# Kernel tuning notes

Hardware: AMD Instinct MI355X
Metric: run time of the kernel (lower is better)

## Reference

```python
import jax, jax.numpy as jnp
import numpy as np

DEPTH = 2
DIM = 256
MLP = 1024
B = 2
N = 2048


def setup_inputs() -> dict:
    key = jax.random.key(0)
    ks = jax.random.split(key, 6)
    s = 0.02
    d = DIM
    f32 = jnp.float32
    return {
        "x": jax.random.normal(ks[0], (B, N, d), f32),
        "ln1_g": jnp.ones((DEPTH, d), f32),
        "ln1_b": jnp.zeros((DEPTH, d), f32),
        "Wqkv": (jax.random.normal(ks[1], (DEPTH, d, 3 * d), f32) * s),
        "bqkv": jnp.zeros((DEPTH, 3 * d), f32),
        "Wo": (jax.random.normal(ks[2], (DEPTH, d, d), f32) * s),
        "bo": jnp.zeros((DEPTH, d), f32),
        "ln2_g": jnp.ones((DEPTH, d), f32),
        "ln2_b": jnp.zeros((DEPTH, d), f32),
        "W1": (jax.random.normal(ks[3], (DEPTH, d, MLP), f32) * s),
        "b1": jnp.zeros((DEPTH, MLP), f32),
        "W2": (jax.random.normal(ks[4], (DEPTH, MLP, d), f32) * s),
        "b2": jnp.zeros((DEPTH, d), f32),
        "heads": 8,
    }


def _ln(x, g, b, eps=1e-5):
    m = x.mean(-1, keepdims=True)
    v = ((x - m) ** 2).mean(-1, keepdims=True)
    return (x - m) * jax.lax.rsqrt(v + eps) * g + b


def reference(x, ln1_g, ln1_b, Wqkv, bqkv, Wo, bo, ln2_g, ln2_b, W1, b1, W2, b2, heads):
    b, n, dim = x.shape
    hd = dim // heads
    scale = hd ** -0.5
    depth = Wqkv.shape[0]
    out = x
    # NOTE: faithful to original: `x` is never updated inside the loop,
    # so only the last layer's output is returned.
    for i in range(depth):
        y = _ln(x, ln1_g[i], ln1_b[i])
        qkv = y @ Wqkv[i] + bqkv[i]                      # [b,n,3*dim]
        qkv = qkv.reshape(b, n, 3, heads, hd)
        q, k, v = jnp.moveaxis(qkv, 2, 0)                # each [b,n,h,hd]
        q = q.transpose(0, 2, 1, 3)                      # [b,h,n,hd]
        k = k.transpose(0, 2, 1, 3)
        v = v.transpose(0, 2, 1, 3)
        dots = jnp.einsum('bhid,bhjd->bhij', q, k) * scale
        attn = jax.nn.softmax(dots, axis=-1)
        o = jnp.einsum('bhij,bhjd->bhid', attn, v)       # [b,h,n,hd]
        o = o.transpose(0, 2, 1, 3).reshape(b, n, dim)
        o = o @ Wo[i] + bo[i]
        a = o + x                                        # attn residual
        z = _ln(a, ln2_g[i], ln2_b[i])
        m = jax.nn.gelu(z @ W1[i] + b1[i], approximate=False) @ W2[i] + b2[i]
        out = m + a                                      # mlp residual
    return out
```

## Files before the change

kernel.cpp:

```cpp
#include <hip/hip_runtime.h>
#include <hip/hip_bf16.h>
#include <math.h>

#define DEPTHC 2
#define DIMD   256
#define MLPD   1024
#define BB     2
#define NN     2048
#define HH     8
#define HD     32
#define ROWS   (BB * NN)

typedef __attribute__((ext_vector_type(8))) short bf16x8;
typedef __attribute__((ext_vector_type(4))) float f32x4;

__device__ __forceinline__ short f2bf(float x) {
    union { float f; unsigned u; } c; c.f = x;
    unsigned u = c.u + (0x7fffu + ((c.u >> 16) & 1u));
    return (short)(u >> 16);
}
__device__ __forceinline__ float bf2f(short s) {
    union { unsigned u; float f; } c; c.u = ((unsigned)(unsigned short)s) << 16;
    return c.f;
}

__global__ __launch_bounds__(256) void prep(
    const float* __restrict__ Wqkv, const float* __restrict__ Wo,
    const float* __restrict__ W1,   const float* __restrict__ W2,
    short* __restrict__ WqkvF, short* __restrict__ WoF,
    short* __restrict__ W1F,   short* __restrict__ W2F,
    const float* __restrict__ x, const float* __restrict__ g,
    const float* __restrict__ be, short* __restrict__ y)
{
    __shared__ short Ts[128][72];

    if (blockIdx.x >= 96) {
        const int wave = threadIdx.x >> 6;
        const int lane = threadIdx.x & 63;
        const int row  = (blockIdx.x - 96) * 4 + wave;
        const int c    = lane * 4;

        const float4 v = *(const float4*)&x[(size_t)row * DIMD + c];
        float s  = v.x + v.y + v.z + v.w;
        float sq = v.x * v.x + v.y * v.y + v.z * v.z + v.w * v.w;
#pragma unroll
        for (int off = 32; off > 0; off >>= 1) {
            s  += __shfl_down(s,  off, 64);
            sq += __shfl_down(sq, off, 64);
        }
        s  = __shfl(s,  0, 64);
        sq = __shfl(sq, 0, 64);

        const float mean = s * (1.f / DIMD);
        const float var  = sq * (1.f / DIMD) - mean * mean;
        const float rstd = rsqrtf(var + 1e-5f);

        const float4 gg = *(const float4*)&g[c];
        const float4 bb = *(const float4*)&be[c];
        short4 ov;
        ov.x = f2bf((v.x - mean) * rstd * gg.x + bb.x);
        ov.y = f2bf((v.y - mean) * rstd * gg.y + bb.y);
        ov.z = f2bf((v.z - mean) * rstd * gg.z + bb.z);
        ov.w = f2bf((v.w - mean) * rstd * gg.w + bb.w);
        *(short4*)&y[(size_t)row * DIMD + c] = ov;
        return;
    }

    int blk = blockIdx.x;
    const float* W; short* WF; int K, N;
    if (blk < 24)      {           W = Wqkv; WF = WqkvF; K = 256;  N = 768;  }
    else if (blk < 32) { blk -= 24; W = Wo;   WF = WoF;   K = 256;  N = 256;  }
    else if (blk < 64) { blk -= 32; W = W1;   WF = W1F;   K = 256;  N = 1024; }
    else               { blk -= 64; W = W2;   WF = W2F;   K = 1024; N = 256;  }
    const int nkc = K >> 7;
    const int bx  = blk / nkc;
    const int kc  = blk % nkc;
    const int n0  = bx * 64;
    const int k0  = kc * 128;

    const int nc  = threadIdx.x & 63;
    const int kr0 = threadIdx.x >> 6;
#pragma unroll
    for (int i = 0; i < 32; ++i) {
        const int kr = kr0 + i * 4;
        Ts[kr][nc] = f2bf(W[(size_t)(k0 + kr) * N + n0 + nc]);
    }
    __syncthreads();

    short* out = WF + ((size_t)bx * nkc + kc) * 8192;
#pragma unroll
    for (int i = 0; i < 4; ++i) {
        const int u    = threadIdx.x + i * 256;
        const int l16  = u & 15;
        const int quad = (u >> 4) & 3;
        const int nt   = (u >> 6) & 3;
        const int ks   = (u >> 8) & 3;
        const int n    = nt * 16 + l16;
        const int kk   = (ks * 4 + quad) * 8;
        bf16x8 v;
#pragma unroll
        for (int j = 0; j < 8; ++j) v[j] = Ts[kk + j][n];
        *(bf16x8*)&out[(size_t)u * 8] = v;
    }
}

template <int K, bool GELU, bool RES, bool OBF, bool VTG>
__global__ __launch_bounds__(256) void gemm_ks(
    const short* __restrict__ A, const short* __restrict__ WF,
    const float* __restrict__ bias, const float* __restrict__ R,
    void* __restrict__ Cv, int N, short* __restrict__ vtg)
{
    __shared__ short smem[4][4096];

    const int tid  = threadIdx.x;
    const int w    = tid >> 6;
    const int lane = tid & 63;
    const int quad = lane >> 4;
    const int l16  = lane & 15;
    const int n0   = blockIdx.x * 64;
    const int m0   = blockIdx.y * 64;
    constexpr int NKC   = K / 128;
    constexpr int SLICE = K / 4;
    constexpr int NHC   = SLICE / 64;

    const short* wfb  = WF + (size_t)blockIdx.x * NKC * 8192;
    const short* arow = A + (size_t)(m0 + l16) * K + quad * 8;
    short* reg = smem[w];

    f32x4 acc[4][4] = {};

#pragma unroll
    for (int hc = 0; hc < NHC; ++hc) {
        const int kbase = w * SLICE + hc * 64;
        const short* src = wfb +
            ((size_t)(kbase >> 7) * 1024 + (size_t)((kbase >> 6) & 1) * 512) * 8;
#pragma unroll
        for (int i = 0; i < 8; ++i)
            *(bf16x8*)&reg[(i * 64 + lane) * 8] =
                *(const bf16x8*)&src[(size_t)(i * 64 + lane) * 8];

#pragma unroll
        for (int ksl = 0; ksl < 2; ++ksl) {
            const int kk = kbase + ksl * 32;
            bf16x8 af[4];
#pragma unroll
            for (int mt = 0; mt < 4; ++mt)
                af[mt] = *(const bf16x8*)(arow + (size_t)mt * 16 * K + kk);
#pragma unroll
            for (int nt = 0; nt < 4; ++nt) {
                const bf16x8 bf = *(const bf16x8*)
                    &reg[(((ksl * 4 + nt) * 4 + quad) * 16 + l16) * 8];
#pragma unroll
                for (int mt = 0; mt < 4; ++mt)
                    acc[mt][nt] = __builtin_amdgcn_mfma_f32_16x16x32_bf16(
                        af[mt], bf, acc[mt][nt], 0, 0, 0);
            }
        }
    }

#pragma unroll
    for (int p = 0; p < 2; ++p) {
        __syncthreads();
#pragma unroll
        for (int mtl = 0; mtl < 2; ++mtl)
#pragma unroll
            for (int nt = 0; nt < 4; ++nt)
                *(f32x4*)&smem[w][((mtl * 4 + nt) * 64 + lane) * 8] = acc[2 * p + mtl][nt];
        __syncthreads();
        if ((w >> 1) == p) {
            const int mtl = w & 1;
            const int mt  = 2 * p + mtl;
#pragma unroll
            for (int nt = 0; nt < 4; ++nt) {
                const int idx = ((mtl * 4 + nt) * 64 + lane) * 8;
                const f32x4 s0 = *(const f32x4*)&smem[0][idx];
                const f32x4 s1 = *(const f32x4*)&smem[1][idx];
                const f32x4 s2 = *(const f32x4*)&smem[2][idx];
                const f32x4 s3 = *(const f32x4*)&smem[3][idx];
                const f32x4 s  = (s0 + s1) + (s2 + s3);
                const int col  = n0 + nt * 16 + l16;
                const float bb = bias[col];
#pragma unroll
                for (int r = 0; r < 4; ++r) {
                    const int row = m0 + mt * 16 + quad * 4 + r;
                    float v = s[r] + bb;
                    if (RES)  v += R[(size_t)row * N + col];
                    if (GELU) v = 0.5f * v * (1.f + erff(v * 0.70710678118f));
                    const short bv = f2bf(v);
                    if (OBF) ((short*)Cv)[(size_t)row * N + col] = bv;
                    else     ((float*)Cv)[(size_t)row * N + col] = v;
                    if (VTG && n0 >= 2 * DIMD) {
                        const int vc = col - 2 * DIMD;
                        const int b  = row >> 11;
                        const int q  = row & (NN - 1);
                        const int h  = vc >> 5;
                        const int d  = vc & 31;
                        vtg[((size_t)(b * HH + h) * HD + d) * NN + q] = bv;
                    }
                }
            }
        }
    }
}

__global__ __launch_bounds__(256) void attn_mfma(
    const short* __restrict__ qkv, const short* __restrict__ vtg,
    short* __restrict__ o)
{
    __shared__ __align__(16) short Ks2[2][64][40];
    __shared__ __align__(16) short Vs2[2][32][72];
    __shared__ __align__(16) short Ps[4][16][72];

    const int tid  = threadIdx.x;
    const int w    = tid >> 6;
    const int lane = tid & 63;
    const int quad = lane >> 4;
    const int l16  = lane & 15;
    const int qw    = w & 1;
    const int kside = w >> 1;
    const int bh   = blockIdx.y;
    const int b    = bh >> 3;
    const int h    = bh & 7;
    const int q0   = blockIdx.x * 32 + qw * 16;

    const float scale = 0.17677669529663689f;
    const float shift = 11.090354888959125f;
    const short* base = qkv + (size_t)b * NN * (3 * DIMD);

    const bf16x8 qfrag =
        *(const bf16x8*)(base + (size_t)(q0 + l16) * (3 * DIMD) + h * HD + quad * 8);

    const int side = tid >> 7;
    const int st   = tid & 127;
    const int kr   = st >> 1;
    const int kd   = (st & 1) * 16;
    const int vd   = st >> 2;
    const int vk0  = (st & 3) * 16;

    const short* kgp = base + (size_t)(side * 1024 + kr) * (3 * DIMD)
                       + DIMD + h * HD + kd;
    const short* vgp = vtg + ((size_t)bh * HD + vd) * NN + side * 1024 + vk0;

    f32x4 oacc0 = {0.f, 0.f, 0.f, 0.f};
    f32x4 oacc1 = {0.f, 0.f, 0.f, 0.f};
    float rowsum = 0.f;

    bf16x8 kr0 = *(const bf16x8*)kgp;
    bf16x8 kr1 = *(const bf16x8*)(kgp + 8);
    bf16x8 vr0 = *(const bf16x8*)vgp;
    bf16x8 vr1 = *(const bf16x8*)(vgp + 8);

#pragma unroll 1
    for (int t = 0; t < NN / 128; ++t) {
        __syncthreads();
        *(bf16x8*)&Ks2[side][kr][kd]     = kr0;
        *(bf16x8*)&Ks2[side][kr][kd + 8] = kr1;
        *(bf16x8*)&Vs2[side][vd][vk0]     = vr0;
        *(bf16x8*)&Vs2[side][vd][vk0 + 8] = vr1;
        __syncthreads();

        if (t + 1 < NN / 128) {
            const short* kn = kgp + (size_t)(t + 1) * 64 * (3 * DIMD);
            const short* vn = vgp + (t + 1) * 64;
            kr0 = *(const bf16x8*)kn;
            kr1 = *(const bf16x8*)(kn + 8);
            vr0 = *(const bf16x8*)vn;
            vr1 = *(const bf16x8*)(vn + 8);
        }

        f32x4 s[4];
#pragma unroll
        for (int kt = 0; kt < 4; ++kt) {
            const bf16x8 kf = *(const bf16x8*)&Ks2[kside][kt * 16 + l16][quad * 8];
            f32x4 z = {0.f, 0.f, 0.f, 0.f};
            s[kt] = __builtin_amdgcn_mfma_f32_16x16x32_bf16(kf, qfrag, z, 0, 0, 0);
        }

#pragma unroll
        for (int kt = 0; kt < 4; ++kt) {
            short4 pv;
#pragma unroll
            for (int r = 0; r < 4; ++r) {
                const float p = __expf(fmaf(s[kt][r], scale, -shift));
                rowsum += p;
                union { float f; unsigned u; } cv; cv.f = p;
                ((short*)&pv)[r] = (short)(cv.u >> 16);
            }
            *(short4*)&Ps[w][l16][kt * 16 + quad * 4] = pv;
        }

#pragma unroll
        for (int c = 0; c < 2; ++c) {
            const bf16x8 pf = *(const bf16x8*)&Ps[w][l16][c * 32 + quad * 8];
            const bf16x8 v0 = *(const bf16x8*)&Vs2[kside][l16][c * 32 + quad * 8];
            const bf16x8 v1 = *(const bf16x8*)&Vs2[kside][16 + l16][c * 32 + quad * 8];
            oacc0 = __builtin_amdgcn_mfma_f32_16x16x32_bf16(pf, v0, oacc0, 0, 0, 0);
            oacc1 = __builtin_amdgcn_mfma_f32_16x16x32_bf16(pf, v1, oacc1, 0, 0, 0);
        }
    }

    rowsum += __shfl_xor(rowsum, 16, 64);
    rowsum += __shfl_xor(rowsum, 32, 64);

    float* sc = (float*)&Ks2[0][0][0];
    __syncthreads();
    if (kside == 1) {
        float* o8 = sc + (size_t)(qw * 64 + lane) * 8;
        *(f32x4*)o8       = oacc0;
        *(f32x4*)(o8 + 4) = oacc1;
        if (lane < 16) sc[1024 + qw * 16 + lane] = rowsum;
    }
    __syncthreads();
    if (kside == 0) {
        const float* o8 = sc + (size_t)(qw * 64 + lane) * 8;
        oacc0 += *(const f32x4*)o8;
        oacc1 += *(const f32x4*)(o8 + 4);
        rowsum += sc[1024 + qw * 16 + l16];

#pragma unroll
        for (int r = 0; r < 4; ++r) {
            const float L   = __shfl(rowsum, quad * 4 + r, 16);
            const float inv = 1.f / L;
            const size_t row = (size_t)(b * NN + q0 + quad * 4 + r);
            o[row * DIMD + h * HD + l16]      = f2bf(oacc0[r] * inv);
            o[row * DIMD + h * HD + 16 + l16] = f2bf(oacc1[r] * inv);
        }
    }
}

__global__ __launch_bounds__(256) void tail_fused(
    const short* __restrict__ obf, const float* __restrict__ x,
    const short* __restrict__ WoF, const float* __restrict__ bo,
    const float* __restrict__ ln2g, const float* __restrict__ ln2b,
    const short* __restrict__ W1F, const float* __restrict__ b1,
    const short* __restrict__ W2F, const float* __restrict__ b2,
    float* __restrict__ out)
{
    __shared__ __align__(16) float aS[16][260];
    __shared__ __align__(16) short zS[16][264];
    __shared__ __align__(16) short mS[16][1032];

    const int tid  = threadIdx.x;
    const int w    = tid >> 6;
    const int lane = tid & 63;
    const int quad = lane >> 4;
    const int l16  = lane & 15;
    const int m0   = blockIdx.x * 16;

    {
        const short* arow   = obf + (size_t)(m0 + l16) * DIMD + quad * 8;
        const short* wchunk = WoF + (size_t)w * 2 * 8192;
        f32x4 acc[4] = {};
#pragma unroll
        for (int ks = 0; ks < 8; ++ks) {
            const int k = ks * 32;
            const bf16x8 af = *(const bf16x8*)(arow + k);
            const int ub = (k >> 7) * 1024 + ((k >> 5) & 3) * 256 + quad * 16 + l16;
#pragma unroll
            for (int nt = 0; nt < 4; ++nt) {
                const bf16x8 bf = *(const bf16x8*)&wchunk[(size_t)(ub + nt * 64) * 8];
                acc[nt] = __builtin_amdgcn_mfma_f32_16x16x32_bf16(af, bf, acc[nt], 0, 0, 0);
            }
        }
#pragma unroll
        for (int nt = 0; nt < 4; ++nt) {
            const int col  = w * 64 + nt * 16 + l16;
            const float bb = bo[col];
#pragma unroll
            for (int r = 0; r < 4; ++r) {
                const int row = quad * 4 + r;
                aS[row][col] = acc[nt][r] + bb + x[(size_t)(m0 + row) * DIMD + col];
            }
        }
    }
    __syncthreads();

    {
        const int row = tid >> 4;
        const int seg = (tid & 15) * 16;
        float s = 0.f, sq = 0.f;
#pragma unroll
        for (int i = 0; i < 16; ++i) {
            const float v = aS[row][seg + i];
            s += v; sq += v * v;
        }
#pragma unroll
        for (int off = 1; off < 16; off <<= 1) {
            s  += __shfl_xor(s,  off, 64);
            sq += __shfl_xor(sq, off, 64);
        }
        const float mean = s * (1.f / DIMD);
        const float var  = sq * (1.f / DIMD) - mean * mean;
        const float rstd = rsqrtf(var + 1e-5f);
#pragma unroll
        for (int i = 0; i < 16; ++i) {
            const int c = seg + i;
            zS[row][c] = f2bf((aS[row][c] - mean) * rstd * ln2g[c] + ln2b[c]);
        }
    }
    __syncthreads();

    {
        f32x4 acc[16] = {};
#pragma unroll
        for (int ks = 0; ks < 8; ++ks) {
            const int k = ks * 32;
            const bf16x8 af = *(const bf16x8*)&zS[l16][k + quad * 8];
            const int ub = (k >> 7) * 1024 + ((k >> 5) & 3) * 256 + quad * 16 + l16;
#pragma unroll
            for (int nt = 0; nt < 16; ++nt) {
                const int bx = w * 4 + (nt >> 2);
                const bf16x8 bf = *(const bf16x8*)
                    &W1F[(size_t)bx * 2 * 8192 + (size_t)(ub + (nt & 3) * 64) * 8];
                acc[nt] = __builtin_amdgcn_mfma_f32_16x16x32_bf16(af, bf, acc[nt], 0, 0, 0);
            }
        }
#pragma unroll
        for (int nt = 0; nt < 16; ++nt) {
            const int col  = w * 256 + nt * 16 + l16;
            const float bb = b1[col];
#pragma unroll
            for (int r = 0; r < 4; ++r) {
                float v = acc[nt][r] + bb;
                v = 0.5f * v * (1.f + erff(v * 0.70710678118f));
                mS[quad * 4 + r][col] = f2bf(v);
            }
        }
    }
    __syncthreads();

    {
        f32x4 acc[4] = {};
        const short* wchunk = W2F + (size_t)w * 8 * 8192;
#pragma unroll
        for (int ks = 0; ks < 32; ++ks) {
            const int k = ks * 32;
            const bf16x8 af = *(const bf16x8*)&mS[l16][k + quad * 8];
            const int ub = (k >> 7) * 1024 + ((k >> 5) & 3) * 256 + quad * 16 + l16;
#pragma unroll
            for (int nt = 0; nt < 4; ++nt) {
                const bf16x8 bf = *(const bf16x8*)&wchunk[(size_t)(ub + nt * 64) * 8];
                acc[nt] = __builtin_amdgcn_mfma_f32_16x16x32_bf16(af, bf, acc[nt], 0, 0, 0);
            }
        }
#pragma unroll
        for (int nt = 0; nt < 4; ++nt) {
            const int col  = w * 64 + nt * 16 + l16;
            const float bb = b2[col];
#pragma unroll
            for (int r = 0; r < 4; ++r) {
                const int row = quad * 4 + r;
                out[(size_t)(m0 + row) * DIMD + col] = acc[nt][r] + bb + aS[row][col];
            }
        }
    }
}

extern "C" void kernel_launch(void* const* d_in, const int* in_sizes, int n_in,
                              void* d_out, int out_size, void* d_ws, size_t ws_size,
                              hipStream_t stream)
{
    const int L = DEPTHC - 1;
    const float* x     = (const float*)d_in[0];
    const float* ln1_g = (const float*)d_in[1]  + L * DIMD;
    const float* ln1_b = (const float*)d_in[2]  + L * DIMD;
    const float* Wqkv  = (const float*)d_in[3]  + (size_t)L * DIMD * 3 * DIMD;
    const float* bqkv  = (const float*)d_in[4]  + L * 3 * DIMD;
    const float* Wo    = (const float*)d_in[5]  + (size_t)L * DIMD * DIMD;
    const float* bo    = (const float*)d_in[6]  + L * DIMD;
    const float* ln2_g = (const float*)d_in[7]  + L * DIMD;
    const float* ln2_b = (const float*)d_in[8]  + L * DIMD;
    const float* W1    = (const float*)d_in[9]  + (size_t)L * DIMD * MLPD;
    const float* b1    = (const float*)d_in[10] + L * MLPD;
    const float* W2    = (const float*)d_in[11] + (size_t)L * MLPD * DIMD;
    const float* b2    = (const float*)d_in[12] + L * DIMD;
    float* out = (float*)d_out;

    short* WqkvF = (short*)d_ws;
    short* WoF   = WqkvF + 12 * 2 * 8192;
    short* W1F   = WoF   + 4 * 2 * 8192;
    short* W2F   = W1F   + 16 * 2 * 8192;
    short* ybf   = W2F   + 4 * 8 * 8192;
    short* qkvbf = ybf   + (size_t)ROWS * DIMD;
    short* vtg   = qkvbf + (size_t)ROWS * 3 * DIMD;
    short* obf   = vtg   + (size_t)16 * HD * NN;

    prep<<<96 + ROWS / 4, 256, 0, stream>>>(
        Wqkv, Wo, W1, W2, WqkvF, WoF, W1F, W2F, x, ln1_g, ln1_b, ybf);

    gemm_ks<256, false, false, true, true><<<dim3(12, 64), 256, 0, stream>>>(
        ybf, WqkvF, bqkv, nullptr, qkvbf, 3 * DIMD, vtg);

    attn_mfma<<<dim3(NN / 32, BB * HH), 256, 0, stream>>>(qkvbf, vtg, obf);

    tail_fused<<<ROWS / 16, 256, 0, stream>>>(
        obf, x, WoF, bo, ln2_g, ln2_b, W1F, b1, W2F, b2, out);
}
```

Before: 157.8 us.

## Stage V transpose through LDS and widen tail kernel to 16 waves

```diff
diff --git a/kernel.cpp b/kernel.cpp
--- a/kernel.cpp
+++ b/kernel.cpp
@@ -111,6 +111,7 @@
     void* __restrict__ Cv, int N, short* __restrict__ vtg)
 {
     __shared__ short smem[4][4096];
+    __shared__ short vts[64][66];
 
     const int tid  = threadIdx.x;
     const int w    = tid >> 6;
@@ -189,17 +190,28 @@
                     const short bv = f2bf(v);
                     if (OBF) ((short*)Cv)[(size_t)row * N + col] = bv;
                     else     ((float*)Cv)[(size_t)row * N + col] = v;
-                    if (VTG && n0 >= 2 * DIMD) {
-                        const int vc = col - 2 * DIMD;
-                        const int b  = row >> 11;
-                        const int q  = row & (NN - 1);
-                        const int h  = vc >> 5;
-                        const int d  = vc & 31;
-                        vtg[((size_t)(b * HH + h) * HD + d) * NN + q] = bv;
-                    }
+                    if (VTG && n0 >= 2 * DIMD)
+                        vts[row - m0][col - n0] = bv;
                 }
             }
         }
+    }
+
+    if (VTG && n0 >= 2 * DIMD) {
+        __syncthreads();
+        const int vcol = tid >> 2;
+        const int tseg = (tid & 3) * 16;
+        const int vc   = n0 - 2 * DIMD + vcol;
+        const int b    = m0 >> 11;
+        const int q0v  = m0 & (NN - 1);
+        const int h    = vc >> 5;
+        const int d    = vc & 31;
+        short tmp[16];
+#pragma unroll
+        for (int i = 0; i < 16; ++i) tmp[i] = vts[tseg + i][vcol];
+        short* dst = &vtg[((size_t)(b * HH + h) * HD + d) * NN + q0v + tseg];
+        *(bf16x8*)dst       = *(const bf16x8*)&tmp[0];
+        *(bf16x8*)(dst + 8) = *(const bf16x8*)&tmp[8];
     }
 }
 
@@ -328,7 +340,7 @@
     }
 }
 
-__global__ __launch_bounds__(256) void tail_fused(
+__global__ __launch_bounds__(1024) void tail_fused(
     const short* __restrict__ obf, const float* __restrict__ x,
     const short* __restrict__ WoF, const float* __restrict__ bo,
     const float* __restrict__ ln2g, const float* __restrict__ ln2b,
@@ -336,7 +348,7 @@
     const short* __restrict__ W2F, const float* __restrict__ b2,
     float* __restrict__ out)
 {
-    __shared__ __align__(16) float aS[16][260];
+    __shared__ __align__(16) float aS[16][264];
     __shared__ __align__(16) short zS[16][264];
     __shared__ __align__(16) short mS[16][1032];
 
@@ -349,75 +361,69 @@
 
     {
         const short* arow   = obf + (size_t)(m0 + l16) * DIMD + quad * 8;
-        const short* wchunk = WoF + (size_t)w * 2 * 8192;
-        f32x4 acc[4] = {};
+        const short* wchunk = WoF + (size_t)(w >> 2) * 2 * 8192;
+        const int ntl = w & 3;
+        f32x4 acc = {};
 #pragma unroll
         for (int ks = 0; ks < 8; ++ks) {
             const int k = ks * 32;
             const bf16x8 af = *(const bf16x8*)(arow + k);
             const int ub = (k >> 7) * 1024 + ((k >> 5) & 3) * 256 + quad * 16 + l16;
-#pragma unroll
-            for (int nt = 0; nt < 4; ++nt) {
-                const bf16x8 bf = *(const bf16x8*)&wchunk[(size_t)(ub + nt * 64) * 8];
-                acc[nt] = __builtin_amdgcn_mfma_f32_16x16x32_bf16(af, bf, acc[nt], 0, 0, 0);
-            }
-        }
-#pragma unroll
-        for (int nt = 0; nt < 4; ++nt) {
-            const int col  = w * 64 + nt * 16 + l16;
-            const float bb = bo[col];
-#pragma unroll
-            for (int r = 0; r < 4; ++r) {
-                const int row = quad * 4 + r;
-                aS[row][col] = acc[nt][r] + bb + x[(size_t)(m0 + row) * DIMD + col];
-            }
+            const bf16x8 bf = *(const bf16x8*)&wchunk[(size_t)(ub + ntl * 64) * 8];
+            acc = __builtin_amdgcn_mfma_f32_16x16x32_bf16(af, bf, acc, 0, 0, 0);
+        }
+        const int col  = w * 16 + l16;
+        const float bb = bo[col];
+#pragma unroll
+        for (int r = 0; r < 4; ++r) {
+            const int row = quad * 4 + r;
+            aS[row][col] = acc[r] + bb + x[(size_t)(m0 + row) * DIMD + col];
         }
     }
     __syncthreads();
 
     {
-        const int row = tid >> 4;
-        const int seg = (tid & 15) * 16;
-        float s = 0.f, sq = 0.f;
-#pragma unroll
-        for (int i = 0; i < 16; ++i) {
-            const float v = aS[row][seg + i];
-            s += v; sq += v * v;
-        }
-#pragma unroll
-        for (int off = 1; off < 16; off <<= 1) {
+        const int row = w;
+        const int c4  = lane * 4;
+        const float4 v = *(const float4*)&aS[row][c4];
+        float s  = v.x + v.y + v.z + v.w;
+        float sq = v.x * v.x + v.y * v.y + v.z * v.z + v.w * v.w;
+#pragma unroll
+        for (int off = 32; off > 0; off >>= 1) {
             s  += __shfl_xor(s,  off, 64);
             sq += __shfl_xor(sq, off, 64);
         }
         const float mean = s * (1.f / DIMD);
         const float var  = sq * (1.f / DIMD) - mean * mean;
         const float rstd = rsqrtf(var + 1e-5f);
-#pragma unroll
-        for (int i = 0; i < 16; ++i) {
-            const int c = seg + i;
-            zS[row][c] = f2bf((aS[row][c] - mean) * rstd * ln2g[c] + ln2b[c]);
-        }
+        const float4 gg = *(const float4*)&ln2g[c4];
+        const float4 bb = *(const float4*)&ln2b[c4];
+        short4 ov;
+        ov.x = f2bf((v.x - mean) * rstd * gg.x + bb.x);
+        ov.y = f2bf((v.y - mean) * rstd * gg.y + bb.y);
+        ov.z = f2bf((v.z - mean) * rstd * gg.z + bb.z);
+        ov.w = f2bf((v.w - mean) * rstd * gg.w + bb.w);
+        *(short4*)&zS[row][c4] = ov;
     }
     __syncthreads();
 
     {
-        f32x4 acc[16] = {};
+        f32x4 acc[4] = {};
 #pragma unroll
         for (int ks = 0; ks < 8; ++ks) {
             const int k = ks * 32;
             const bf16x8 af = *(const bf16x8*)&zS[l16][k + quad * 8];
             const int ub = (k >> 7) * 1024 + ((k >> 5) & 3) * 256 + quad * 16 + l16;
 #pragma unroll
-            for (int nt = 0; nt < 16; ++nt) {
-                const int bx = w * 4 + (nt >> 2);
+            for (int nt = 0; nt < 4; ++nt) {
                 const bf16x8 bf = *(const bf16x8*)
-                    &W1F[(size_t)bx * 2 * 8192 + (size_t)(ub + (nt & 3) * 64) * 8];
+                    &W1F[(size_t)w * 2 * 8192 + (size_t)(ub + nt * 64) * 8];
                 acc[nt] = __builtin_amdgcn_mfma_f32_16x16x32_bf16(af, bf, acc[nt], 0, 0, 0);
             }
         }
 #pragma unroll
-        for (int nt = 0; nt < 16; ++nt) {
-            const int col  = w * 256 + nt * 16 + l16;
+        for (int nt = 0; nt < 4; ++nt) {
+            const int col  = w * 64 + nt * 16 + l16;
             const float bb = b1[col];
 #pragma unroll
             for (int r = 0; r < 4; ++r) {
@@ -430,28 +436,23 @@
     __syncthreads();
 
     {
-        f32x4 acc[4] = {};
-        const short* wchunk = W2F + (size_t)w * 8 * 8192;
+        f32x4 acc = {};
+        const short* wchunk = W2F + (size_t)(w >> 2) * 8 * 8192;
+        const int ntl = w & 3;
 #pragma unroll
         for (int ks = 0; ks < 32; ++ks) {
             const int k = ks * 32;
             const bf16x8 af = *(const bf16x8*)&mS[l16][k + quad * 8];
             const int ub = (k >> 7) * 1024 + ((k >> 5) & 3) * 256 + quad * 16 + l16;
-#pragma unroll
-            for (int nt = 0; nt < 4; ++nt) {
-                const bf16x8 bf = *(const bf16x8*)&wchunk[(size_t)(ub + nt * 64) * 8];
-                acc[nt] = __builtin_amdgcn_mfma_f32_16x16x32_bf16(af, bf, acc[nt], 0, 0, 0);
-            }
-        }
-#pragma unroll
-        for (int nt = 0; nt < 4; ++nt) {
-            const int col  = w * 64 + nt * 16 + l16;
-            const float bb = b2[col];
-#pragma unroll
-            for (int r = 0; r < 4; ++r) {
-                const int row = quad * 4 + r;
-                out[(size_t)(m0 + row) * DIMD + col] = acc[nt][r] + bb + aS[row][col];
-            }
+            const bf16x8 bf = *(const bf16x8*)&wchunk[(size_t)(ub + ntl * 64) * 8];
+            acc = __builtin_amdgcn_mfma_f32_16x16x32_bf16(af, bf, acc, 0, 0, 0);
+        }
+        const int col  = w * 16 + l16;
+        const float bb = b2[col];
+#pragma unroll
+        for (int r = 0; r < 4; ++r) {
+            const int row = quad * 4 + r;
+            out[(size_t)(m0 + row) * DIMD + col] = acc[r] + bb + aS[row][col];
         }
     }
 }
@@ -493,6 +494,6 @@
 
     attn_mfma<<<dim3(NN / 32, BB * HH), 256, 0, stream>>>(qkvbf, vtg, obf);
 
-    tail_fused<<<ROWS / 16, 256, 0, stream>>>(
+    tail_fused<<<ROWS / 16, 1024, 0, stream>>>(
         obf, x, WoF, bo, ln2_g, ln2_b, W1F, b1, W2F, b2, out);
 }
```

Measured after the change: 141.5 us. -10.3%, faster.
